# Optimization experiments

Hardware: AMD Instinct MI355X
Metric: run time of the kernel (lower is better)

Reference implementation:

```python
import jax, jax.numpy as jnp
import numpy as np

B, N, I, H = 4, 325, 64, 128
LN_EPS = 1e-5

def setup_inputs() -> dict:
    key = jax.random.key(0)
    ks = jax.random.split(key, 20)
    x = jax.random.normal(ks[0], (B, N, I), dtype=jnp.float32)
    # sparse binary adjacency with self-loops (as the module masks adj == 0)
    a = (jax.random.uniform(ks[1], (B, N, N)) < 0.05).astype(jnp.float32)
    adj = jnp.maximum(a, jnp.eye(N, dtype=jnp.float32)[None])
    h = jax.random.normal(ks[2], (B, N, H), dtype=jnp.float32)
    c = jax.random.normal(ks[3], (B, N, H), dtype=jnp.float32)
    def glorot(k, shape):
        fan_in, fan_out = shape[-1], shape[0]
        s = jnp.sqrt(2.0 / (fan_in + fan_out)).astype(jnp.float32)
        return jax.random.normal(k, shape, dtype=jnp.float32) * s
    params = {
        'W_ih': glorot(ks[4], (4 * H, I)),
        'W_hh': glorot(ks[5], (4 * H, H)),
        'b_ih': jnp.zeros((4 * H,), jnp.float32),
        'b_hh': jnp.zeros((4 * H,), jnp.float32),
        'gc_w': glorot(ks[6], (H, H)),
        'gc_b': jnp.zeros((H,), jnp.float32),
        'Ws_w': glorot(ks[7], (H, H)),
        'Ws_b': jnp.zeros((H,), jnp.float32),
        'Wt_w': glorot(ks[8], (H, H)),
        'Wt_b': jnp.zeros((H,), jnp.float32),
        'v': glorot(ks[9], (H, 1)),
        'ln_g': jnp.ones((H,), jnp.float32),
        'ln_b': jnp.zeros((H,), jnp.float32),
        'comb_w': glorot(ks[10], (H, 2 * H)),
        'comb_b': jnp.zeros((H,), jnp.float32),
    }
    return {'x': x, 'adj': adj, 'h': h, 'c': c, **params}


def reference(x, adj, h, c, W_ih, W_hh, b_ih, b_hh, gc_w, gc_b,
              Ws_w, Ws_b, Wt_w, Wt_b, v, ln_g, ln_b, comb_w, comb_b):
    # --- LSTMCell applied per node (PyTorch gate order: i, f, g, o) ---
    gates = (jnp.einsum('bni,gi->bng', x, W_ih) + b_ih
             + jnp.einsum('bnh,gh->bng', h, W_hh) + b_hh)  # [B,N,4H]
    i_g, f_g, g_g, o_g = jnp.split(gates, 4, axis=-1)
    c_lstm = jax.nn.sigmoid(f_g) * c + jax.nn.sigmoid(i_g) * jnp.tanh(g_g)
    h_lstm = jax.nn.sigmoid(o_g) * jnp.tanh(c_lstm)  # [B,N,H]
    # --- Graph convolution: adj @ (h W) + b ---
    support = jnp.einsum('bnh,ho->bno', h_lstm, gc_w)
    h_graph = jnp.einsum('bnm,bmo->bno', adj, support) + gc_b
    # --- Spatial attention (tanh-additive, adjacency-masked softmax) ---
    s = jnp.einsum('bnh,oh->bno', h_graph, Ws_w) + Ws_b  # W_s(x)
    t = jnp.einsum('bnh,oh->bno', h_graph, Wt_w) + Wt_b  # W_t(x)
    # scores[b,i,j] = tanh(s[b,i] + t[b,j]) @ v ; big [B,N,N,H] intermediate
    scores = jnp.einsum('bijh,h->bij',
                        jnp.tanh(s[:, :, None, :] + t[:, None, :, :]),
                        v[:, 0])
    scores = jnp.where(adj == 0, -1e9, scores)
    attn = jax.nn.softmax(scores, axis=-1)
    context = jnp.einsum('bij,bjh->bih', attn, h_graph)
    # --- LayerNorm ---
    mu = jnp.mean(context, axis=-1, keepdims=True)
    var = jnp.var(context, axis=-1, keepdims=True)
    h_att = ln_g * (context - mu) * jax.lax.rsqrt(var + LN_EPS) + ln_b
    # --- Combine ---
    h_comb = jnp.concatenate([h_lstm, h_att], axis=-1)
    h_new = jnp.einsum('bnk,ok->bno', h_comb, comb_w) + comb_b
    return (h_new, c_lstm)
```

## Files before the change

### kernel.cpp

```cpp
#include <hip/hip_runtime.h>

#define B_ 4
#define N_ 325
#define I_ 64
#define H_ 128
#define NODES (B_ * N_)
#define NZMAX 64

typedef unsigned short u16;
typedef unsigned int u32;

__device__ __align__(16) float g_WT   [192 * 512];
__device__ __align__(16) float g_gcw  [128 * 128];
__device__ __align__(16) float g_WsT  [128 * 128];
__device__ __align__(16) float g_WtT  [128 * 128];
__device__ __align__(16) float g_combT[256 * 128];
__device__ float g_bias[512];
__device__ float g_svec[896];

__device__ __align__(16) float g_support[(size_t)NODES * H_];
__device__ __align__(16) float g_h_graph[(size_t)NODES * H_];
__device__ __align__(16) float g_s_buf  [(size_t)NODES * H_];
__device__ __align__(16) float g_t_buf  [(size_t)NODES * H_];
__device__ __align__(16) float g_hl     [(size_t)NODES * H_];
__device__ u16 g_nz [(size_t)NODES * NZMAX];
__device__ int g_nzc[NODES];

__device__ __forceinline__ float bf2f(u16 u) { return __uint_as_float(((u32)u) << 16); }
__device__ __forceinline__ u16 f2bf(float f) {
    u32 u = __float_as_uint(f);
    u += 0x7fffu + ((u >> 16) & 1u);
    return (u16)(u >> 16);
}
__device__ __forceinline__ float ldin(const void* p, size_t i, int f32) {
    return f32 ? ((const float*)p)[i] : bf2f(((const u16*)p)[i]);
}
__device__ __forceinline__ void stout(void* p, size_t i, float v, int f32) {
    if (f32) ((float*)p)[i] = v; else ((u16*)p)[i] = f2bf(v);
}
__device__ __forceinline__ float fast_rcp(float x) { return __builtin_amdgcn_rcpf(x); }
__device__ __forceinline__ float sigm(float x) { return fast_rcp(1.f + __expf(-x)); }
__device__ __forceinline__ float tanh_f(float x) {
    x = fminf(15.f, fmaxf(-15.f, x));
    float e = __expf(2.f * x);
    return (e - 1.f) * fast_rcp(e + 1.f);
}
__device__ __forceinline__ int probe_f32(const void* adj) {
    return ((((const u32*)adj)[0] & 0xFFFFu) != 0x3F80u) ? 1 : 0;
}

__global__ __launch_bounds__(256) void k0_prep(
    const void* __restrict__ W_ih, const void* __restrict__ W_hh,
    const void* __restrict__ b_ih, const void* __restrict__ b_hh,
    const void* __restrict__ gc_w, const void* __restrict__ gc_b,
    const void* __restrict__ Ws_w, const void* __restrict__ Ws_b,
    const void* __restrict__ Wt_w, const void* __restrict__ Wt_b,
    const void* __restrict__ vvec, const void* __restrict__ ln_g,
    const void* __restrict__ ln_b, const void* __restrict__ comb_w,
    const void* __restrict__ comb_b, const void* __restrict__ adj)
{
    const int f32 = probe_f32(adj);
    const int b = blockIdx.x;
    const int t = threadIdx.x;
    if (b < 40) {
        __shared__ float tile[64][65];
        const void* src; float* dst;
        int C, r0, c0, dstStride, dstRowOff;
        if (b < 8)       { src = W_ih;   dst = g_WT;    C = 64;  r0 = b * 64;            c0 = 0;              dstStride = 512; dstRowOff = 0;  }
        else if (b < 24) { int i = b - 8;  src = W_hh;   dst = g_WT;    C = 128; r0 = (i >> 1) * 64; c0 = (i & 1) * 64;  dstStride = 512; dstRowOff = 64; }
        else if (b < 28) { int i = b - 24; src = Ws_w;   dst = g_WsT;   C = 128; r0 = (i >> 1) * 64; c0 = (i & 1) * 64;  dstStride = 128; dstRowOff = 0;  }
        else if (b < 32) { int i = b - 28; src = Wt_w;   dst = g_WtT;   C = 128; r0 = (i >> 1) * 64; c0 = (i & 1) * 64;  dstStride = 128; dstRowOff = 0;  }
        else             { int i = b - 32; src = comb_w; dst = g_combT; C = 256; r0 = (i >> 2) * 64; c0 = (i & 3) * 64;  dstStride = 128; dstRowOff = 0;  }
        const int lane = t & 63, wv = t >> 6;
        for (int rr = wv; rr < 64; rr += 4)
            tile[rr][lane] = ldin(src, (size_t)(r0 + rr) * C + c0 + lane, f32);
        __syncthreads();
        for (int cc = wv; cc < 64; cc += 4)
            dst[(size_t)(dstRowOff + c0 + cc) * dstStride + r0 + lane] = tile[lane][cc];
    } else {
        for (int e = (b - 40) * 256 + t; e < 16384 + 512 + 896; e += 8 * 256) {
            if (e < 16384) { g_gcw[e] = ldin(gc_w, e, f32); }
            else if (e < 16896) {
                const int i = e - 16384;
                g_bias[i] = ldin(b_ih, i, f32) + ldin(b_hh, i, f32);
            } else {
                const int i = e - 16896;
                const int seg = i >> 7, k = i & 127;
                const void* s = (seg == 0) ? gc_b : (seg == 1) ? Ws_b : (seg == 2) ? Wt_b :
                                (seg == 3) ? vvec : (seg == 4) ? ln_g : (seg == 5) ? ln_b : comb_b;
                g_svec[i] = ldin(s, k, f32);
            }
        }
    }
}

__global__ __launch_bounds__(256) void k1_lstm(
    const void* __restrict__ x, const void* __restrict__ h, const void* __restrict__ c,
    const void* __restrict__ adj, void* __restrict__ out)
{
    const int f32 = probe_f32(adj);
    __shared__ __align__(8) float2 xh2[192];
    __shared__ __align__(8) float2 Gt2[512];
    __shared__ __align__(8) float2 hl2[128];
    const int node0 = blockIdx.x * 2;
    const int t = threadIdx.x;

    for (int e = t; e < 384; e += 256) {
        const int n = e / 192, k = e % 192;
        const int node = node0 + n;
        ((float*)&xh2[k])[n] = (k < 64) ? ldin(x, (size_t)node * 64 + k, f32)
                                        : ldin(h, (size_t)node * 128 + (k - 64), f32);
    }
    __syncthreads();

    {
        float a0 = 0.f, a1 = 0.f, b0 = 0.f, b1 = 0.f;
        #pragma unroll 8
        for (int k = 0; k < 192; ++k) {
            const float w0 = g_WT[(size_t)k * 512 + t];
            const float w1 = g_WT[(size_t)k * 512 + t + 256];
            const float2 xv = xh2[k];
            a0 = fmaf(xv.x, w0, a0); a1 = fmaf(xv.y, w0, a1);
            b0 = fmaf(xv.x, w1, b0); b1 = fmaf(xv.y, w1, b1);
        }
        const float bi0 = g_bias[t], bi1 = g_bias[t + 256];
        Gt2[t]       = make_float2(a0 + bi0, a1 + bi0);
        Gt2[t + 256] = make_float2(b0 + bi1, b1 + bi1);
    }
    __syncthreads();

    {
        const int n = t >> 7, hh = t & 127;
        const int node = node0 + n;
        const float ig = ((const float*)&Gt2[hh])[n];
        const float fg = ((const float*)&Gt2[128 + hh])[n];
        const float gv = ((const float*)&Gt2[256 + hh])[n];
        const float og = ((const float*)&Gt2[384 + hh])[n];
        const float cl = sigm(fg) * ldin(c, (size_t)node * 128 + hh, f32) + sigm(ig) * tanh_f(gv);
        const float hv = sigm(og) * tanh_f(cl);
        stout(out, (size_t)(NODES * H_) + (size_t)node * 128 + hh, cl, f32);
        g_hl[(size_t)node * 128 + hh] = hv;
        ((float*)&hl2[hh])[n] = hv;
    }
    __syncthreads();

    {
        const int o = t & 127, n = t >> 7;
        float acc = 0.f;
        #pragma unroll 8
        for (int k = 0; k < 128; ++k)
            acc = fmaf(((const float*)&hl2[k])[n], g_gcw[(size_t)k * 128 + o], acc);
        g_support[(size_t)(node0 + n) * 128 + o] = acc;
    }
}

__global__ __launch_bounds__(256) void k2_graph(const void* __restrict__ adj)
{
    const int f32 = probe_f32(adj);
    __shared__ __align__(16) float4 hg4[128];
    __shared__ u16 nzi[4][NZMAX];
    __shared__ float nzv[4][NZMAX];
    __shared__ int cnt[4];
    const int node0 = blockIdx.x * 4;
    const int t = threadIdx.x;
    const int lane = t & 63, w = t >> 6;

    if (t < 4) cnt[t] = 0;
    __syncthreads();
    for (int j = lane; j < N_; j += 64) {
        float a = ldin(adj, (size_t)(node0 + w) * N_ + j, f32);
        if (a != 0.f) {
            int p = atomicAdd(&cnt[w], 1);
            if (p < NZMAX) { nzi[w][p] = (u16)j; nzv[w][p] = a; }
        }
    }
    __syncthreads();
    if (t < 4) g_nzc[node0 + t] = min(cnt[t], NZMAX);
    #pragma unroll
    for (int n = 0; n < 4; ++n) {
        const int cnn = min(cnt[n], NZMAX);
        for (int p = t; p < cnn; p += 256) g_nz[(size_t)(node0 + n) * NZMAX + p] = nzi[n][p];
    }

    const int o = t & 127;
    const float gb = g_svec[o];
    #pragma unroll
    for (int ps = 0; ps < 2; ++ps) {
        const int n = (t >> 7) + 2 * ps;
        const int node = node0 + n;
        const int bn = node / N_;
        const int cnn = min(cnt[n], NZMAX);
        float acc = gb;
        for (int p = 0; p < cnn; ++p)
            acc = fmaf(nzv[n][p], g_support[((size_t)bn * N_ + nzi[n][p]) * 128 + o], acc);
        g_h_graph[(size_t)node * 128 + o] = acc;
        ((float*)&hg4[o])[n] = acc;
    }
    __syncthreads();

    {
        const int which = t >> 7;
        const float* WT = which ? g_WtT : g_WsT;
        const float bias = g_svec[128 + which * 128 + o];
        float a0 = 0.f, a1 = 0.f, a2 = 0.f, a3 = 0.f;
        #pragma unroll 8
        for (int k = 0; k < 128; ++k) {
            const float wv = WT[(size_t)k * 128 + o];
            const float4 hv = hg4[k];
            a0 = fmaf(hv.x, wv, a0); a1 = fmaf(hv.y, wv, a1);
            a2 = fmaf(hv.z, wv, a2); a3 = fmaf(hv.w, wv, a3);
        }
        float* dst = which ? g_t_buf : g_s_buf;
        dst[(size_t)(node0 + 0) * 128 + o] = a0 + bias;
        dst[(size_t)(node0 + 1) * 128 + o] = a1 + bias;
        dst[(size_t)(node0 + 2) * 128 + o] = a2 + bias;
        dst[(size_t)(node0 + 3) * 128 + o] = a3 + bias;
    }
}

__global__ __launch_bounds__(256) void k3_attn(
    const void* __restrict__ adj, void* __restrict__ out)
{
    const int f32 = probe_f32(adj);
    __shared__ __align__(16) float4 comb4[256];
    __shared__ float s_i[4][H_];
    __shared__ float red[4][H_];
    __shared__ float nzs[4][NZMAX];
    __shared__ u16 nzi[4][NZMAX];
    __shared__ float part[2][4][H_];
    __shared__ float mu_[4], rstd_[4], smv[4];
    __shared__ int cnt[4];
    const int node0 = blockIdx.x * 4;
    const int t = threadIdx.x;
    const int lane = t & 63, w = t >> 6;

    if (t < 4) cnt[t] = g_nzc[node0 + t];
    for (int e = t; e < 512; e += 256) {
        const int n = e >> 7, k = e & 127;
        const int node = node0 + n;
        s_i[n][k] = g_s_buf[(size_t)node * 128 + k];
        ((float*)&comb4[k])[n] = g_hl[(size_t)node * 128 + k];
    }
    __syncthreads();
    #pragma unroll
    for (int n = 0; n < 4; ++n)
        for (int p = t; p < cnt[n]; p += 256) nzi[n][p] = g_nz[(size_t)(node0 + n) * NZMAX + p];
    __syncthreads();

    {
        const int bn = (node0 + w) / N_;
        const int cn = cnt[w];
        const float v0 = g_svec[384 + lane], v1 = g_svec[384 + 64 + lane];
        const float si0 = s_i[w][lane], si1 = s_i[w][lane + 64];
        for (int p = 0; p < cn; ++p) {
            const float* tj = g_t_buf + ((size_t)bn * N_ + nzi[w][p]) * 128;
            float a = v0 * tanh_f(si0 + tj[lane]) + v1 * tanh_f(si1 + tj[lane + 64]);
            #pragma unroll
            for (int off = 32; off > 0; off >>= 1) a += __shfl_xor(a, off);
            if (lane == 0) nzs[w][p] = a;
        }
    }
    __syncthreads();

    if (t < 4) {
        const int cn = cnt[t];
        float m = -1e30f;
        for (int p = 0; p < cn; ++p) m = fmaxf(m, nzs[t][p]);
        float ssum = 0.f;
        for (int p = 0; p < cn; ++p) { float e = __expf(nzs[t][p] - m); nzs[t][p] = e; ssum += e; }
        smv[t] = fast_rcp(ssum);
    }
    __syncthreads();

    const int o = t & 127;
    #pragma unroll
    for (int ps = 0; ps < 2; ++ps) {
        const int n = (t >> 7) + 2 * ps;
        const int bn = (node0 + n) / N_;
        const int cn = cnt[n];
        float acc = 0.f;
        for (int p = 0; p < cn; ++p)
            acc = fmaf(nzs[n][p], g_h_graph[((size_t)bn * N_ + nzi[n][p]) * 128 + o], acc);
        red[n][o] = acc * smv[n];
    }
    __syncthreads();

    {
        float x0 = red[w][lane], x1 = red[w][lane + 64];
        float sm = x0 + x1, sq = x0 * x0 + x1 * x1;
        #pragma unroll
        for (int off = 32; off > 0; off >>= 1) {
            sm += __shfl_xor(sm, off);
            sq += __shfl_xor(sq, off);
        }
        if (lane == 0) {
            float mu = sm * (1.f / H_);
            float var = fmaxf(sq * (1.f / H_) - mu * mu, 0.f);
            mu_[w] = mu;
            rstd_[w] = __builtin_amdgcn_rsqf(var + 1e-5f);
        }
    }
    __syncthreads();
    for (int e = t; e < 512; e += 256) {
        const int n = e >> 7, k = e & 127;
        float xn = (red[n][k] - mu_[n]) * rstd_[n];
        ((float*)&comb4[128 + k])[n] = g_svec[512 + k] * xn + g_svec[640 + k];
    }
    __syncthreads();

    {
        const int half = t >> 7;
        float a0 = 0.f, a1 = 0.f, a2 = 0.f, a3 = 0.f;
        const int k0 = half * 128;
        #pragma unroll 8
        for (int kk = 0; kk < 128; ++kk) {
            const float wv = g_combT[(size_t)(k0 + kk) * 128 + o];
            const float4 cv = comb4[k0 + kk];
            a0 = fmaf(cv.x, wv, a0); a1 = fmaf(cv.y, wv, a1);
            a2 = fmaf(cv.z, wv, a2); a3 = fmaf(cv.w, wv, a3);
        }
        part[half][0][o] = a0; part[half][1][o] = a1;
        part[half][2][o] = a2; part[half][3][o] = a3;
    }
    __syncthreads();
    for (int e = t; e < 512; e += 256) {
        const int n = e >> 7, k = e & 127;
        stout(out, (size_t)(node0 + n) * 128 + k,
              part[0][n][k] + part[1][n][k] + g_svec[768 + k], f32);
    }
}

extern "C" void kernel_launch(void* const* d_in, const int* in_sizes, int n_in,
                              void* d_out, int out_size, void* d_ws, size_t ws_size,
                              hipStream_t stream)
{
    (void)in_sizes; (void)n_in; (void)out_size; (void)d_ws; (void)ws_size;
    const void* x      = d_in[0];
    const void* adj    = d_in[1];
    const void* h      = d_in[2];
    const void* c      = d_in[3];
    const void* W_ih   = d_in[4];
    const void* W_hh   = d_in[5];
    const void* b_ih   = d_in[6];
    const void* b_hh   = d_in[7];
    const void* gc_w   = d_in[8];
    const void* gc_b   = d_in[9];
    const void* Ws_w   = d_in[10];
    const void* Ws_b   = d_in[11];
    const void* Wt_w   = d_in[12];
    const void* Wt_b   = d_in[13];
    const void* vvec   = d_in[14];
    const void* ln_g   = d_in[15];
    const void* ln_b   = d_in[16];
    const void* comb_w = d_in[17];
    const void* comb_b = d_in[18];

    k0_prep <<<48, 256, 0, stream>>>(W_ih, W_hh, b_ih, b_hh, gc_w, gc_b,
                                     Ws_w, Ws_b, Wt_w, Wt_b, vvec, ln_g, ln_b,
                                     comb_w, comb_b, adj);
    k1_lstm <<<NODES / 2, 256, 0, stream>>>(x, h, c, adj, d_out);
    k2_graph<<<NODES / 4, 256, 0, stream>>>(adj);
    k3_attn <<<NODES / 4, 256, 0, stream>>>(adj, d_out);
}
```

Measured before the change: 155.7 us.

## Process four nodes per LSTM block and add ILP to sparse gathers

The LSTM kernel now runs 512-thread blocks that each handle four nodes. Every weight load from g_WT is reused across four nodes instead of two, which halves total weight traffic. The sparse aggregation loops in the graph and attention kernels use two independent accumulators to expose more memory-level parallelism. The attention score loop also splits each wavefront into two half-waves that score two neighbours at once with a shorter shuffle reduction. The trade-offs are fewer LSTM blocks (325) and more registers per thread.

```diff
diff --git a/kernel.cpp b/kernel.cpp
--- a/kernel.cpp
+++ b/kernel.cpp
@@ -94,53 +94,52 @@
     }
 }
 
-__global__ __launch_bounds__(256) void k1_lstm(
+__global__ __launch_bounds__(512) void k1_lstm(
     const void* __restrict__ x, const void* __restrict__ h, const void* __restrict__ c,
     const void* __restrict__ adj, void* __restrict__ out)
 {
     const int f32 = probe_f32(adj);
-    __shared__ __align__(8) float2 xh2[192];
-    __shared__ __align__(8) float2 Gt2[512];
-    __shared__ __align__(8) float2 hl2[128];
-    const int node0 = blockIdx.x * 2;
+    __shared__ __align__(16) float4 xh4[192];
+    __shared__ __align__(16) float4 Gt4[512];
+    __shared__ __align__(16) float4 hl4[128];
+    const int node0 = blockIdx.x * 4;
     const int t = threadIdx.x;
 
-    for (int e = t; e < 384; e += 256) {
+    for (int e = t; e < 768; e += 512) {
         const int n = e / 192, k = e % 192;
         const int node = node0 + n;
-        ((float*)&xh2[k])[n] = (k < 64) ? ldin(x, (size_t)node * 64 + k, f32)
+        ((float*)&xh4[k])[n] = (k < 64) ? ldin(x, (size_t)node * 64 + k, f32)
                                         : ldin(h, (size_t)node * 128 + (k - 64), f32);
     }
     __syncthreads();
 
     {
-        float a0 = 0.f, a1 = 0.f, b0 = 0.f, b1 = 0.f;
+        const int g = t;
+        float a0 = 0.f, a1 = 0.f, a2 = 0.f, a3 = 0.f;
         #pragma unroll 8
         for (int k = 0; k < 192; ++k) {
-            const float w0 = g_WT[(size_t)k * 512 + t];
-            const float w1 = g_WT[(size_t)k * 512 + t + 256];
-            const float2 xv = xh2[k];
-            a0 = fmaf(xv.x, w0, a0); a1 = fmaf(xv.y, w0, a1);
-            b0 = fmaf(xv.x, w1, b0); b1 = fmaf(xv.y, w1, b1);
-        }
-        const float bi0 = g_bias[t], bi1 = g_bias[t + 256];
-        Gt2[t]       = make_float2(a0 + bi0, a1 + bi0);
-        Gt2[t + 256] = make_float2(b0 + bi1, b1 + bi1);
+            const float wv = g_WT[(size_t)k * 512 + g];
+            const float4 xv = xh4[k];
+            a0 = fmaf(xv.x, wv, a0); a1 = fmaf(xv.y, wv, a1);
+            a2 = fmaf(xv.z, wv, a2); a3 = fmaf(xv.w, wv, a3);
+        }
+        const float bias = g_bias[g];
+        Gt4[g] = make_float4(a0 + bias, a1 + bias, a2 + bias, a3 + bias);
     }
     __syncthreads();
 
     {
         const int n = t >> 7, hh = t & 127;
         const int node = node0 + n;
-        const float ig = ((const float*)&Gt2[hh])[n];
-        const float fg = ((const float*)&Gt2[128 + hh])[n];
-        const float gv = ((const float*)&Gt2[256 + hh])[n];
-        const float og = ((const float*)&Gt2[384 + hh])[n];
+        const float ig = ((const float*)&Gt4[hh])[n];
+        const float fg = ((const float*)&Gt4[128 + hh])[n];
+        const float gv = ((const float*)&Gt4[256 + hh])[n];
+        const float og = ((const float*)&Gt4[384 + hh])[n];
         const float cl = sigm(fg) * ldin(c, (size_t)node * 128 + hh, f32) + sigm(ig) * tanh_f(gv);
         const float hv = sigm(og) * tanh_f(cl);
         stout(out, (size_t)(NODES * H_) + (size_t)node * 128 + hh, cl, f32);
         g_hl[(size_t)node * 128 + hh] = hv;
-        ((float*)&hl2[hh])[n] = hv;
+        ((float*)&hl4[hh])[n] = hv;
     }
     __syncthreads();
 
@@ -149,7 +148,7 @@
         float acc = 0.f;
         #pragma unroll 8
         for (int k = 0; k < 128; ++k)
-            acc = fmaf(((const float*)&hl2[k])[n], g_gcw[(size_t)k * 128 + o], acc);
+            acc = fmaf(((const float*)&hl4[k])[n], g_gcw[(size_t)k * 128 + o], acc);
         g_support[(size_t)(node0 + n) * 128 + o] = acc;
     }
 }
@@ -190,9 +189,15 @@
         const int node = node0 + n;
         const int bn = node / N_;
         const int cnn = min(cnt[n], NZMAX);
-        float acc = gb;
-        for (int p = 0; p < cnn; ++p)
-            acc = fmaf(nzv[n][p], g_support[((size_t)bn * N_ + nzi[n][p]) * 128 + o], acc);
+        float accA = 0.f, accB = 0.f;
+        int p = 0;
+        for (; p + 1 < cnn; p += 2) {
+            accA = fmaf(nzv[n][p],     g_support[((size_t)bn * N_ + nzi[n][p])     * 128 + o], accA);
+            accB = fmaf(nzv[n][p + 1], g_support[((size_t)bn * N_ + nzi[n][p + 1]) * 128 + o], accB);
+        }
+        if (p < cnn)
+            accA = fmaf(nzv[n][p], g_support[((size_t)bn * N_ + nzi[n][p]) * 128 + o], accA);
+        const float acc = accA + accB + gb;
         g_h_graph[(size_t)node * 128 + o] = acc;
         ((float*)&hg4[o])[n] = acc;
     }
@@ -250,14 +255,22 @@
     {
         const int bn = (node0 + w) / N_;
         const int cn = cnt[w];
-        const float v0 = g_svec[384 + lane], v1 = g_svec[384 + 64 + lane];
-        const float si0 = s_i[w][lane], si1 = s_i[w][lane + 64];
-        for (int p = 0; p < cn; ++p) {
-            const float* tj = g_t_buf + ((size_t)bn * N_ + nzi[w][p]) * 128;
-            float a = v0 * tanh_f(si0 + tj[lane]) + v1 * tanh_f(si1 + tj[lane + 64]);
-            #pragma unroll
-            for (int off = 32; off > 0; off >>= 1) a += __shfl_xor(a, off);
-            if (lane == 0) nzs[w][p] = a;
+        const int sl = lane & 31, hf = lane >> 5;
+        const float v0 = g_svec[384 + sl],      v1 = g_svec[384 + 32 + sl];
+        const float v2 = g_svec[384 + 64 + sl], v3 = g_svec[384 + 96 + sl];
+        const float s0 = s_i[w][sl],      s1 = s_i[w][sl + 32];
+        const float s2 = s_i[w][sl + 64], s3 = s_i[w][sl + 96];
+        for (int base = 0; base < cn; base += 2) {
+            const int p = base + hf;
+            float a = 0.f;
+            if (p < cn) {
+                const float* tj = g_t_buf + ((size_t)bn * N_ + nzi[w][p]) * 128;
+                a = v0 * tanh_f(s0 + tj[sl])      + v1 * tanh_f(s1 + tj[sl + 32])
+                  + v2 * tanh_f(s2 + tj[sl + 64]) + v3 * tanh_f(s3 + tj[sl + 96]);
+            }
+            a += __shfl_xor(a, 16); a += __shfl_xor(a, 8);
+            a += __shfl_xor(a, 4);  a += __shfl_xor(a, 2); a += __shfl_xor(a, 1);
+            if (sl == 0 && p < cn) nzs[w][p] = a;
         }
     }
     __syncthreads();
@@ -278,10 +291,15 @@
         const int n = (t >> 7) + 2 * ps;
         const int bn = (node0 + n) / N_;
         const int cn = cnt[n];
-        float acc = 0.f;
-        for (int p = 0; p < cn; ++p)
-            acc = fmaf(nzs[n][p], g_h_graph[((size_t)bn * N_ + nzi[n][p]) * 128 + o], acc);
-        red[n][o] = acc * smv[n];
+        float accA = 0.f, accB = 0.f;
+        int p = 0;
+        for (; p + 1 < cn; p += 2) {
+            accA = fmaf(nzs[n][p],     g_h_graph[((size_t)bn * N_ + nzi[n][p])     * 128 + o], accA);
+            accB = fmaf(nzs[n][p + 1], g_h_graph[((size_t)bn * N_ + nzi[n][p + 1]) * 128 + o], accB);
+        }
+        if (p < cn)
+            accA = fmaf(nzs[n][p], g_h_graph[((size_t)bn * N_ + nzi[n][p]) * 128 + o], accA);
+        red[n][o] = (accA + accB) * smv[n];
     }
     __syncthreads();
 
@@ -358,7 +376,7 @@
     k0_prep <<<48, 256, 0, stream>>>(W_ih, W_hh, b_ih, b_hh, gc_w, gc_b,
                                      Ws_w, Ws_b, Wt_w, Wt_b, vvec, ln_g, ln_b,
                                      comb_w, comb_b, adj);
-    k1_lstm <<<NODES / 2, 256, 0, stream>>>(x, h, c, adj, d_out);
+    k1_lstm <<<NODES / 4, 512, 0, stream>>>(x, h, c, adj, d_out);
     k2_graph<<<NODES / 4, 256, 0, stream>>>(adj);
     k3_attn <<<NODES / 4, 256, 0, stream>>>(adj, d_out);
 }
```

New measurement: 151.6 us. 1.03x faster.
